# Kernel optimization log

Hardware: AMD Instinct MI355X
Metric: run time of the kernel (lower is better)

The kernel has to match this reference:

```python
import jax, jax.numpy as jnp
import numpy as np

TOKEN_DIM = 512
ATTN_DIM = 512
NUM_HEADS = 8
MLP_SIZE = 2048
EPS = 1e-6


def setup_inputs() -> dict:
    key = jax.random.key(0)
    ks = jax.random.split(key, 9)
    s_tok = 1.0 / np.sqrt(TOKEN_DIM)
    s_att = 1.0 / np.sqrt(ATTN_DIM)
    s_mlp = 1.0 / np.sqrt(MLP_SIZE)
    return {
        "inputs": jax.random.normal(ks[0], (2, 4096, TOKEN_DIM), dtype=jnp.float32),
        "Wq": jax.random.uniform(ks[1], (TOKEN_DIM, ATTN_DIM), jnp.float32, -s_tok, s_tok),
        "Wk": jax.random.uniform(ks[2], (TOKEN_DIM, ATTN_DIM), jnp.float32, -s_tok, s_tok),
        "Wv": jax.random.uniform(ks[3], (TOKEN_DIM, ATTN_DIM), jnp.float32, -s_tok, s_tok),
        "Wo": jax.random.uniform(ks[4], (ATTN_DIM, TOKEN_DIM), jnp.float32, -s_att, s_att),
        "W1": jax.random.uniform(ks[5], (TOKEN_DIM, MLP_SIZE), jnp.float32, -s_tok, s_tok),
        "b1": jax.random.uniform(ks[6], (MLP_SIZE,), jnp.float32, -s_tok, s_tok),
        "W2": jax.random.uniform(ks[7], (MLP_SIZE, TOKEN_DIM), jnp.float32, -s_mlp, s_mlp),
        "b2": jax.random.uniform(ks[8], (TOKEN_DIM,), jnp.float32, -s_mlp, s_mlp),
        "ln_att_g": jnp.ones((TOKEN_DIM,), jnp.float32),
        "ln_att_b": jnp.zeros((TOKEN_DIM,), jnp.float32),
        "ln_mlp_g": jnp.ones((TOKEN_DIM,), jnp.float32),
        "ln_mlp_b": jnp.zeros((TOKEN_DIM,), jnp.float32),
    }


def _layernorm(x, g, b):
    mu = jnp.mean(x, axis=-1, keepdims=True)
    var = jnp.mean(jnp.square(x - mu), axis=-1, keepdims=True)
    return (x - mu) * jax.lax.rsqrt(var + EPS) * g + b


def _attention(x, Wq, Wk, Wv, Wo):
    B, N, _ = x.shape
    H, Dh = NUM_HEADS, ATTN_DIM // NUM_HEADS
    # project then split heads: (B, N, H, Dh) -> (B, H, N, Dh)
    q = (x @ Wq).reshape(B, N, H, Dh).transpose(0, 2, 1, 3)
    k = (x @ Wk).reshape(B, N, H, Dh).transpose(0, 2, 1, 3)
    v = (x @ Wv).reshape(B, N, H, Dh).transpose(0, 2, 1, 3)
    scale = Dh ** -0.5
    scores = jnp.einsum("bhnd,bhmd->bhnm", q, k) * scale  # full NxN scores
    attn = jax.nn.softmax(scores, axis=-1)
    out = jnp.einsum("bhnm,bhmd->bhnd", attn, v)
    out = out.transpose(0, 2, 1, 3).reshape(B, N, ATTN_DIM)
    return out @ Wo


def reference(inputs, Wq, Wk, Wv, Wo, W1, b1, W2, b2,
              ln_att_g, ln_att_b, ln_mlp_g, ln_mlp_b):
    x = _layernorm(inputs, ln_att_g, ln_att_b)
    x = _attention(x, Wq, Wk, Wv, Wo)
    y = x + inputs
    z = _layernorm(y, ln_mlp_g, ln_mlp_b)
    z = jax.nn.gelu(z @ W1 + b1, approximate=False) @ W2 + b2
    return z + y
```

## Files before the change

### kernel.cpp

```cpp
#include <hip/hip_runtime.h>
#include <hip/hip_bf16.h>
#include <cmath>


typedef unsigned short u16;
typedef float  f32x4  __attribute__((ext_vector_type(4)));
typedef short  bf16x8 __attribute__((ext_vector_type(8)));
typedef u16    u16x4  __attribute__((ext_vector_type(4)));

#define DEV __device__ __forceinline__
#define AS1(p) ((const __attribute__((address_space(1))) void*)(p))
#define AS3(p) ((__attribute__((address_space(3))) void*)(p))

static constexpr int Mrows = 8192;
static constexpr int Dtok  = 512;
static constexpr int Fmlp  = 2048;
static constexpr float LOG2E = 1.44269504088896340736f;

DEV u16 f2b(float f) {
  union { float f; unsigned u; } v; v.f = f;
  unsigned r = v.u + 0x7fffu + ((v.u >> 16) & 1u);
  return (u16)(r >> 16);
}

DEV unsigned cvtpk(float a, float b) {
  unsigned r;
  asm("v_cvt_pk_bf16_f32 %0, %1, %2" : "=v"(r) : "v"(a), "v"(b));
  return r;
}

DEV void plswap16(unsigned &a, unsigned &b) {
  asm("v_permlane16_swap_b32 %0, %1" : "+v"(a), "+v"(b));
}

DEV float ex2(float x) {
#if __has_builtin(__builtin_amdgcn_exp2f)
  return __builtin_amdgcn_exp2f(x);
#else
  float r; asm("v_exp_f32 %0, %1" : "=v"(r) : "v"(x)); return r;
#endif
}

DEV f32x4 mfma32(bf16x8 a, bf16x8 b, f32x4 c) {
  return __builtin_amdgcn_mfma_f32_16x16x32_bf16(a, b, c, 0, 0, 0);
}

__global__ __launch_bounds__(256) void convert_all(
    const float* __restrict__ Wq, const float* __restrict__ Wk,
    const float* __restrict__ Wv, const float* __restrict__ Wo,
    const float* __restrict__ W1, const float* __restrict__ W2,
    u16* __restrict__ Wqt, u16* __restrict__ Wkt, u16* __restrict__ Wvt,
    u16* __restrict__ Wot, u16* __restrict__ W1t, u16* __restrict__ W2t,
    float qscale) {
  int bid = blockIdx.x;
  const float* src; u16* dst; int K, N; float sc = 1.0f;
  if (bid < 1024)      { src = Wq; dst = Wqt; K = 512;  N = 512;  sc = qscale; }
  else if (bid < 2048) { src = Wk; dst = Wkt; K = 512;  N = 512;  bid -= 1024; }
  else if (bid < 3072) { src = Wv; dst = Wvt; K = 512;  N = 512;  bid -= 2048; }
  else if (bid < 4096) { src = Wo; dst = Wot; K = 512;  N = 512;  bid -= 3072; }
  else if (bid < 8192) { src = W1; dst = W1t; K = 512;  N = 2048; bid -= 4096; }
  else                 { src = W2; dst = W2t; K = 2048; N = 512;  bid -= 8192; }
  const int idx = bid * 256 + threadIdx.x;
  const int k = idx / N, n = idx - k * N;
  dst[(size_t)n * K + k] = f2b(src[idx] * sc);
}

__global__ __launch_bounds__(256) void ln_kernel(const float* __restrict__ x,
                                                 const float* __restrict__ g,
                                                 const float* __restrict__ b,
                                                 u16* __restrict__ o) {
  const int row = blockIdx.x, tid = threadIdx.x;
  float2 v = ((const float2*)(x + (size_t)row * 512))[tid];
  float s = v.x + v.y, ss = v.x * v.x + v.y * v.y;
#pragma unroll
  for (int off = 32; off > 0; off >>= 1) {
    s  += __shfl_down(s, off);
    ss += __shfl_down(ss, off);
  }
  __shared__ float ps[4], pss[4];
  const int wave = tid >> 6, lane = tid & 63;
  if (lane == 0) { ps[wave] = s; pss[wave] = ss; }
  __syncthreads();
  const float S  = ps[0] + ps[1] + ps[2] + ps[3];
  const float SS = pss[0] + pss[1] + pss[2] + pss[3];
  const float mean = S * (1.0f / 512.0f);
  const float var  = SS * (1.0f / 512.0f) - mean * mean;
  const float rstd = rsqrtf(var + 1e-6f);
  const float2 gg = ((const float2*)g)[tid];
  const float2 bb = ((const float2*)b)[tid];
  ushort2 ov;
  ov.x = f2b((v.x - mean) * rstd * gg.x + bb.x);
  ov.y = f2b((v.y - mean) * rstd * gg.y + bb.y);
  ((ushort2*)(o + (size_t)row * 512))[tid] = ov;
}

template <int EPI, int BM>
__global__ __launch_bounds__(256) void gemm_kernel(
    const u16* __restrict__ A, const u16* __restrict__ Bt,
    u16* __restrict__ outb, u16* __restrict__ outbK, u16* __restrict__ outbV,
    float* __restrict__ outf,
    const float* __restrict__ bias, const float* __restrict__ resid,
    int M, int N, int K) {
  __shared__ u16 Al[BM * 32];
  __shared__ u16 Bl[128 * 32];
  constexpr int WM = BM / 2;
  const int tid = threadIdx.x;
  const int wave = tid >> 6, lane = tid & 63;
  const int lhi = lane >> 4, llo = lane & 15;
  const int wr = wave >> 1, wc = wave & 1;
  const int m0 = blockIdx.y * BM, n0 = blockIdx.x * 128;

  f32x4 acc[BM / 32][4] = {};

  for (int k0 = 0; k0 < K; k0 += 32) {
#pragma unroll
    for (int i = 0; i < BM / 64; ++i) {
      const int rb = i * 64 + wave * 16;
      const u16* sa = A + (size_t)(m0 + rb + (lane >> 2)) * K + k0 + (lane & 3) * 8;
      __builtin_amdgcn_global_load_lds(AS1(sa), AS3(&Al[rb * 32]), 16, 0, 0);
    }
#pragma unroll
    for (int i = 0; i < 2; ++i) {
      const int rb = i * 64 + wave * 16;
      const u16* sb = Bt + (size_t)(n0 + rb + (lane >> 2)) * K + k0 + (lane & 3) * 8;
      __builtin_amdgcn_global_load_lds(AS1(sb), AS3(&Bl[rb * 32]), 16, 0, 0);
    }
    __syncthreads();
    bf16x8 af[BM / 32], bfr[4];
#pragma unroll
    for (int mi = 0; mi < BM / 32; ++mi)
      af[mi] = *(const bf16x8*)&Al[(wr * WM + mi * 16 + llo) * 32 + lhi * 8];
#pragma unroll
    for (int ni = 0; ni < 4; ++ni)
      bfr[ni] = *(const bf16x8*)&Bl[(wc * 64 + ni * 16 + llo) * 32 + lhi * 8];
#pragma unroll
    for (int mi = 0; mi < BM / 32; ++mi)
#pragma unroll
      for (int ni = 0; ni < 4; ++ni)
        acc[mi][ni] = __builtin_amdgcn_mfma_f32_16x16x32_bf16(af[mi], bfr[ni],
                                                              acc[mi][ni], 0, 0, 0);
    __syncthreads();
  }

  if constexpr (EPI == 5) {
    if (n0 < 1024) {
      u16* dst = (n0 < 512) ? outb : outbK;
      const int c0 = (n0 & 511) + wc * 64;
#pragma unroll
      for (int mi = 0; mi < BM / 32; ++mi)
#pragma unroll
        for (int r = 0; r < 4; ++r) {
          const size_t grow = (size_t)m0 + wr * WM + mi * 16 + lhi * 4 + r;
#pragma unroll
          for (int ni = 0; ni < 4; ++ni)
            dst[grow * 512 + c0 + ni * 16 + llo] = f2b(acc[mi][ni][r]);
        }
    } else {
      const int bb = m0 >> 12;
      const int nb = (m0 & 4095) + wr * WM + lhi * 4;
#pragma unroll
      for (int mi = 0; mi < BM / 32; ++mi)
#pragma unroll
        for (int ni = 0; ni < 4; ++ni) {
          const int gcol = (n0 - 1024) + wc * 64 + ni * 16 + llo;
          u16x4 pk;
#pragma unroll
          for (int r = 0; r < 4; ++r) pk[r] = f2b(acc[mi][ni][r]);
          u16* dst = outbV + (((size_t)(bb * 8 + (gcol >> 6))) * 64 + (gcol & 63)) * 4096
                           + nb + mi * 16;
          *(u16x4*)dst = pk;
        }
    }
  } else {
#pragma unroll
    for (int mi = 0; mi < BM / 32; ++mi) {
#pragma unroll
      for (int r = 0; r < 4; ++r) {
        const size_t grow = (size_t)m0 + wr * WM + mi * 16 + lhi * 4 + r;
#pragma unroll
        for (int ni = 0; ni < 4; ++ni) {
          const int gcol = n0 + wc * 64 + ni * 16 + llo;
          float v = acc[mi][ni][r];
          if (EPI == 0) {
            outb[grow * N + gcol] = f2b(v);
          } else if (EPI == 1) {
            v += bias[gcol];
            v = 0.5f * v * (1.0f + erff(v * 0.70710678118654752f));
            outb[grow * N + gcol] = f2b(v);
          } else if (EPI == 2) {
            v += resid[grow * N + gcol];
            outf[grow * N + gcol] = v;
          } else {
            v += bias[gcol] + resid[grow * N + gcol];
            outf[grow * N + gcol] = v;
          }
        }
      }
    }
  }
}

__global__ __launch_bounds__(256) void attn_kernel(const u16* __restrict__ Q,
                                                   const u16* __restrict__ Kg,
                                                   const u16* __restrict__ VT,
                                                   u16* __restrict__ O) {
  const int qt = blockIdx.x, bh = blockIdx.y;
  const int b = bh >> 3, h = bh & 7;
  const int tid = threadIdx.x, wave = tid >> 6, lane = tid & 63;
  const int lhi = lane >> 4, llo = lane & 15;

  __shared__ u16 Kl[2][4096];
  __shared__ u16 Vl[2][4096];

  const size_t rowbase = (size_t)b * 4096;
  const int col0 = h * 64;
  const int q0 = qt * 128;

  bf16x8 qf0[2], qf1[2];
  {
    const u16* qp0 = Q + (rowbase + q0 + wave * 32 + llo) * 512 + col0 + lhi * 8;
    qf0[0] = *(const bf16x8*)qp0;
    qf0[1] = *(const bf16x8*)(qp0 + 32);
    const u16* qp1 = qp0 + (size_t)16 * 512;
    qf1[0] = *(const bf16x8*)qp1;
    qf1[1] = *(const bf16x8*)(qp1 + 32);
  }

  const int srow8 = lane >> 3;
  const int kcsw  = ((lane & 7) ^ srow8) * 8;
  const u16* kbase0 = Kg + (rowbase + wave * 16 + srow8) * 512 + col0 + kcsw;
  const u16* kbase1 = kbase0 + (size_t)8 * 512;
  const u16* vbase0 = VT + ((size_t)bh * 64 + wave * 16 + srow8) * 4096 + kcsw;
  const u16* vbase1 = vbase0 + (size_t)8 * 4096;

  const int xr = (llo & 7) << 4;
  const int ka0 = (16 * lhi) ^ xr;
  const int ka1 = (16 * (4 + lhi)) ^ xr;
  const int csig = ((lhi & 1) << 1) | (lhi >> 1);
  const int vb0 = 16 * (csig ^ (llo & 7));
  const int vb1 = 16 * ((csig | 4) ^ (llo & 7));

  const bf16x8 ones = {(short)0x3F80, (short)0x3F80, (short)0x3F80, (short)0x3F80,
                       (short)0x3F80, (short)0x3F80, (short)0x3F80, (short)0x3F80};

  f32x4 o0[4] = {}, o1[4] = {};
  f32x4 o40 = {}, o41 = {};

  auto stage = [&](int kvr, int B) {
    __builtin_amdgcn_global_load_lds(AS1(kbase0 + (size_t)kvr * 512),
                                     AS3(&Kl[B][wave * 1024]), 16, 0, 0);
    __builtin_amdgcn_global_load_lds(AS1(kbase1 + (size_t)kvr * 512),
                                     AS3(&Kl[B][wave * 1024 + 512]), 16, 0, 0);
    __builtin_amdgcn_global_load_lds(AS1(vbase0 + kvr),
                                     AS3(&Vl[B][wave * 1024]), 16, 0, 0);
    __builtin_amdgcn_global_load_lds(AS1(vbase1 + kvr),
                                     AS3(&Vl[B][wave * 1024 + 512]), 16, 0, 0);
  };

  auto packP = [&](const f32x4* stj, bf16x8& Bv0, bf16x8& Bv1) {
    unsigned a0 = cvtpk(ex2(stj[0][0]), ex2(stj[0][1]));
    unsigned a1 = cvtpk(ex2(stj[0][2]), ex2(stj[0][3]));
    unsigned b0 = cvtpk(ex2(stj[1][0]), ex2(stj[1][1]));
    unsigned b1 = cvtpk(ex2(stj[1][2]), ex2(stj[1][3]));
    unsigned c0 = cvtpk(ex2(stj[2][0]), ex2(stj[2][1]));
    unsigned c1 = cvtpk(ex2(stj[2][2]), ex2(stj[2][3]));
    unsigned d0 = cvtpk(ex2(stj[3][0]), ex2(stj[3][1]));
    unsigned d1 = cvtpk(ex2(stj[3][2]), ex2(stj[3][3]));
    plswap16(a0, b0); plswap16(a1, b1);
    plswap16(c0, d0); plswap16(c1, d1);
    union UB { unsigned u[4]; bf16x8 v; } X, Y;
    X.u[0] = a0; X.u[1] = a1; X.u[2] = b0; X.u[3] = b1;
    Y.u[0] = c0; Y.u[1] = c1; Y.u[2] = d0; Y.u[3] = d1;
    Bv0 = X.v; Bv1 = Y.v;
  };

  auto compute = [&](int B) {
    const char* klb = (const char*)&Kl[B][0] + llo * 128;
    const char* vlb = (const char*)&Vl[B][0] + llo * 128;
    f32x4 st0[4], st1[4];
    __builtin_amdgcn_s_setprio(1);
#pragma unroll
    for (int jt = 0; jt < 4; ++jt) {
      bf16x8 kf0 = *(const bf16x8*)(klb + jt * 2048 + ka0);
      bf16x8 kf1 = *(const bf16x8*)(klb + jt * 2048 + ka1);
      f32x4 z0 = {}, z1 = {};
      z0 = mfma32(kf0, qf0[0], z0); z0 = mfma32(kf1, qf0[1], z0);
      z1 = mfma32(kf0, qf1[0], z1); z1 = mfma32(kf1, qf1[1], z1);
      st0[jt] = z0; st1[jt] = z1;
    }
    __builtin_amdgcn_s_setprio(0);
    bf16x8 P00, P01, P10, P11;
    packP(st0, P00, P01);
    packP(st1, P10, P11);
    __builtin_amdgcn_s_setprio(1);
    o40 = mfma32(ones, P00, o40); o40 = mfma32(ones, P01, o40);
    o41 = mfma32(ones, P10, o41); o41 = mfma32(ones, P11, o41);
#pragma unroll
    for (int dt = 0; dt < 4; ++dt) {
      bf16x8 vf0 = *(const bf16x8*)(vlb + dt * 2048 + vb0);
      bf16x8 vf1 = *(const bf16x8*)(vlb + dt * 2048 + vb1);
      o0[dt] = mfma32(vf0, P00, o0[dt]); o0[dt] = mfma32(vf1, P01, o0[dt]);
      o1[dt] = mfma32(vf0, P10, o1[dt]); o1[dt] = mfma32(vf1, P11, o1[dt]);
    }
    __builtin_amdgcn_s_setprio(0);
  };

  stage(0, 0);
  __syncthreads();
  for (int kv0 = 0; kv0 < 4096; kv0 += 128) {
    stage(kv0 + 64, 1);
    compute(0);
    __syncthreads();
    if (kv0 + 128 < 4096) stage(kv0 + 128, 0);
    compute(1);
    __syncthreads();
  }

  {
    const float inv = 1.0f / o40[0];
    u16* op = O + (rowbase + q0 + wave * 32 + llo) * 512 + col0 + 4 * lhi;
#pragma unroll
    for (int dt = 0; dt < 4; ++dt) {
      u16x4 pk;
#pragma unroll
      for (int r = 0; r < 4; ++r) pk[r] = f2b(o0[dt][r] * inv);
      *(u16x4*)(op + dt * 16) = pk;
    }
  }
  {
    const float inv = 1.0f / o41[0];
    u16* op = O + (rowbase + q0 + wave * 32 + 16 + llo) * 512 + col0 + 4 * lhi;
#pragma unroll
    for (int dt = 0; dt < 4; ++dt) {
      u16x4 pk;
#pragma unroll
      for (int r = 0; r < 4; ++r) pk[r] = f2b(o1[dt][r] * inv);
      *(u16x4*)(op + dt * 16) = pk;
    }
  }
}

extern "C" void kernel_launch(void* const* d_in, const int* in_sizes, int n_in,
                              void* d_out, int out_size, void* d_ws, size_t ws_size,
                              hipStream_t stream) {
  const float* inputs = (const float*)d_in[0];
  const float* Wq  = (const float*)d_in[1];
  const float* Wk  = (const float*)d_in[2];
  const float* Wv  = (const float*)d_in[3];
  const float* Wo  = (const float*)d_in[4];
  const float* W1  = (const float*)d_in[5];
  const float* b1  = (const float*)d_in[6];
  const float* W2  = (const float*)d_in[7];
  const float* b2  = (const float*)d_in[8];
  const float* g1  = (const float*)d_in[9];
  const float* be1 = (const float*)d_in[10];
  const float* g2  = (const float*)d_in[11];
  const float* be2 = (const float*)d_in[12];
  float* out = (float*)d_out;

  const int M = Mrows, D = Dtok, F = Fmlp;

  char* w = (char*)d_ws;
  u16* xln  = (u16*)w;  w += (size_t)M * D * 2;
  u16* Qb   = (u16*)w;  w += (size_t)M * D * 2;
  u16* Kb   = (u16*)w;  w += (size_t)M * D * 2;
  u16* VT   = (u16*)w;  w += (size_t)M * D * 2;
  u16* attn = (u16*)w;  w += (size_t)M * D * 2;
  float* y  = (float*)w; w += (size_t)M * D * 4;
  u16* Wqt  = (u16*)w;  w += (size_t)D * D * 2;
  u16* Wkt  = (u16*)w;  w += (size_t)D * D * 2;
  u16* Wvt  = (u16*)w;  w += (size_t)D * D * 2;
  u16* Wot  = (u16*)w;  w += (size_t)D * D * 2;
  u16* W1t  = (u16*)w;  w += (size_t)D * F * 2;
  u16* W2t  = (u16*)w;  w += (size_t)F * D * 2;
  u16* zln = xln;
  u16* h1  = Qb;

  convert_all<<<dim3(12288), 256, 0, stream>>>(Wq, Wk, Wv, Wo, W1, W2,
                                               Wqt, Wkt, Wvt, Wot, W1t, W2t,
                                               0.125f * LOG2E);

  ln_kernel<<<dim3(M), 256, 0, stream>>>(inputs, g1, be1, xln);

  gemm_kernel<5, 128><<<dim3(12, M / 128), 256, 0, stream>>>(
      xln, Wqt, Qb, Kb, VT, nullptr, nullptr, nullptr, M, 512, D);

  attn_kernel<<<dim3(32, 16), 256, 0, stream>>>(Qb, Kb, VT, attn);

  gemm_kernel<2, 64><<<dim3(4, M / 64), 256, 0, stream>>>(
      attn, Wot, nullptr, nullptr, nullptr, y, nullptr, inputs, M, D, D);

  ln_kernel<<<dim3(M), 256, 0, stream>>>(y, g2, be2, zln);

  gemm_kernel<1, 128><<<dim3(16, M / 128), 256, 0, stream>>>(
      zln, W1t, h1, nullptr, nullptr, nullptr, b1, nullptr, M, F, D);
  gemm_kernel<3, 64><<<dim3(4, M / 64), 256, 0, stream>>>(
      h1, W2t, nullptr, nullptr, nullptr, out, b2, y, M, D, F);
}
```

Before: 243.3 us.

## Split attention KV range across two blocks and double-buffer GEMM LDS

The attention kernel now splits the 4096-key range into two halves along a third grid dimension. Each half writes unnormalized partial outputs and row denominators, and a new combine kernel sums them and normalizes. This doubles the attention grid from 512 to 1024 blocks to fill more of the GPU's compute units, at the cost of an extra launch and extra memory traffic for the partials. Separately, the GEMM kernel gains double-buffered LDS staging so the next K-slice loads while the current one computes, which doubles shared memory use.

```diff
diff --git a/kernel.cpp b/kernel.cpp
--- a/kernel.cpp
+++ b/kernel.cpp
@@ -7,6 +7,7 @@
 typedef float  f32x4  __attribute__((ext_vector_type(4)));
 typedef short  bf16x8 __attribute__((ext_vector_type(8)));
 typedef u16    u16x4  __attribute__((ext_vector_type(4)));
+typedef u16    u16x8  __attribute__((ext_vector_type(8)));
 
 #define DEV __device__ __forceinline__
 #define AS1(p) ((const __attribute__((address_space(1))) void*)(p))
@@ -21,6 +22,10 @@
   union { float f; unsigned u; } v; v.f = f;
   unsigned r = v.u + 0x7fffu + ((v.u >> 16) & 1u);
   return (u16)(r >> 16);
+}
+
+DEV float b2f(u16 x) {
+  union { unsigned u; float f; } v; v.u = ((unsigned)x) << 16; return v.f;
 }
 
 DEV unsigned cvtpk(float a, float b) {
@@ -101,8 +106,8 @@
     float* __restrict__ outf,
     const float* __restrict__ bias, const float* __restrict__ resid,
     int M, int N, int K) {
-  __shared__ u16 Al[BM * 32];
-  __shared__ u16 Bl[128 * 32];
+  __shared__ u16 Al[2][BM * 32];
+  __shared__ u16 Bl[2][128 * 32];
   constexpr int WM = BM / 2;
   const int tid = threadIdx.x;
   const int wave = tid >> 6, lane = tid & 63;
@@ -112,33 +117,45 @@
 
   f32x4 acc[BM / 32][4] = {};
 
-  for (int k0 = 0; k0 < K; k0 += 32) {
+  auto stageG = [&](int k0, int Bf) {
 #pragma unroll
     for (int i = 0; i < BM / 64; ++i) {
       const int rb = i * 64 + wave * 16;
       const u16* sa = A + (size_t)(m0 + rb + (lane >> 2)) * K + k0 + (lane & 3) * 8;
-      __builtin_amdgcn_global_load_lds(AS1(sa), AS3(&Al[rb * 32]), 16, 0, 0);
+      __builtin_amdgcn_global_load_lds(AS1(sa), AS3(&Al[Bf][rb * 32]), 16, 0, 0);
     }
 #pragma unroll
     for (int i = 0; i < 2; ++i) {
       const int rb = i * 64 + wave * 16;
       const u16* sb = Bt + (size_t)(n0 + rb + (lane >> 2)) * K + k0 + (lane & 3) * 8;
-      __builtin_amdgcn_global_load_lds(AS1(sb), AS3(&Bl[rb * 32]), 16, 0, 0);
-    }
-    __syncthreads();
+      __builtin_amdgcn_global_load_lds(AS1(sb), AS3(&Bl[Bf][rb * 32]), 16, 0, 0);
+    }
+  };
+
+  auto computeG = [&](int Bf) {
     bf16x8 af[BM / 32], bfr[4];
 #pragma unroll
     for (int mi = 0; mi < BM / 32; ++mi)
-      af[mi] = *(const bf16x8*)&Al[(wr * WM + mi * 16 + llo) * 32 + lhi * 8];
+      af[mi] = *(const bf16x8*)&Al[Bf][(wr * WM + mi * 16 + llo) * 32 + lhi * 8];
 #pragma unroll
     for (int ni = 0; ni < 4; ++ni)
-      bfr[ni] = *(const bf16x8*)&Bl[(wc * 64 + ni * 16 + llo) * 32 + lhi * 8];
+      bfr[ni] = *(const bf16x8*)&Bl[Bf][(wc * 64 + ni * 16 + llo) * 32 + lhi * 8];
 #pragma unroll
     for (int mi = 0; mi < BM / 32; ++mi)
 #pragma unroll
       for (int ni = 0; ni < 4; ++ni)
         acc[mi][ni] = __builtin_amdgcn_mfma_f32_16x16x32_bf16(af[mi], bfr[ni],
                                                               acc[mi][ni], 0, 0, 0);
+  };
+
+  stageG(0, 0);
+  __syncthreads();
+  for (int k0 = 0; k0 < K; k0 += 64) {
+    stageG(k0 + 32, 1);
+    computeG(0);
+    __syncthreads();
+    if (k0 + 64 < K) stageG(k0 + 64, 0);
+    computeG(1);
     __syncthreads();
   }
 
@@ -203,8 +220,10 @@
 __global__ __launch_bounds__(256) void attn_kernel(const u16* __restrict__ Q,
                                                    const u16* __restrict__ Kg,
                                                    const u16* __restrict__ VT,
-                                                   u16* __restrict__ O) {
-  const int qt = blockIdx.x, bh = blockIdx.y;
+                                                   u16* __restrict__ P0,
+                                                   u16* __restrict__ P1,
+                                                   float* __restrict__ den) {
+  const int qt = blockIdx.x, bh = blockIdx.y, z = blockIdx.z;
   const int b = bh >> 3, h = bh & 7;
   const int tid = threadIdx.x, wave = tid >> 6, lane = tid & 63;
   const int lhi = lane >> 4, llo = lane & 15;
@@ -215,6 +234,7 @@
   const size_t rowbase = (size_t)b * 4096;
   const int col0 = h * 64;
   const int q0 = qt * 128;
+  const int kvlo = z * 2048;
 
   bf16x8 qf0[2], qf1[2];
   {
@@ -305,39 +325,60 @@
     __builtin_amdgcn_s_setprio(0);
   };
 
-  stage(0, 0);
+  stage(kvlo, 0);
   __syncthreads();
-  for (int kv0 = 0; kv0 < 4096; kv0 += 128) {
+  for (int kv0 = kvlo; kv0 < kvlo + 2048; kv0 += 128) {
     stage(kv0 + 64, 1);
     compute(0);
     __syncthreads();
-    if (kv0 + 128 < 4096) stage(kv0 + 128, 0);
+    if (kv0 + 128 < kvlo + 2048) stage(kv0 + 128, 0);
     compute(1);
     __syncthreads();
   }
 
+  u16* P = z ? P1 : P0;
   {
-    const float inv = 1.0f / o40[0];
-    u16* op = O + (rowbase + q0 + wave * 32 + llo) * 512 + col0 + 4 * lhi;
+    const int qrow = q0 + wave * 32 + llo;
+    u16* op = P + (rowbase + qrow) * 512 + col0 + 4 * lhi;
 #pragma unroll
     for (int dt = 0; dt < 4; ++dt) {
       u16x4 pk;
 #pragma unroll
-      for (int r = 0; r < 4; ++r) pk[r] = f2b(o0[dt][r] * inv);
+      for (int r = 0; r < 4; ++r) pk[r] = f2b(o0[dt][r]);
       *(u16x4*)(op + dt * 16) = pk;
     }
+    if (lhi == 0) den[(size_t)z * 65536 + bh * 4096 + qrow] = o40[0];
   }
   {
-    const float inv = 1.0f / o41[0];
-    u16* op = O + (rowbase + q0 + wave * 32 + 16 + llo) * 512 + col0 + 4 * lhi;
+    const int qrow = q0 + wave * 32 + 16 + llo;
+    u16* op = P + (rowbase + qrow) * 512 + col0 + 4 * lhi;
 #pragma unroll
     for (int dt = 0; dt < 4; ++dt) {
       u16x4 pk;
 #pragma unroll
-      for (int r = 0; r < 4; ++r) pk[r] = f2b(o1[dt][r] * inv);
+      for (int r = 0; r < 4; ++r) pk[r] = f2b(o1[dt][r]);
       *(u16x4*)(op + dt * 16) = pk;
     }
-  }
+    if (lhi == 0) den[(size_t)z * 65536 + bh * 4096 + qrow] = o41[0];
+  }
+}
+
+__global__ __launch_bounds__(256) void attn_combine(const u16* __restrict__ P0,
+                                                    const u16* __restrict__ P1,
+                                                    const float* __restrict__ den,
+                                                    u16* __restrict__ out) {
+  const int idx = blockIdx.x * 256 + threadIdx.x;
+  const int row = idx >> 6, c0 = (idx & 63) * 8;
+  const int bq = row & 4095, bb = row >> 12, h = c0 >> 6;
+  const size_t dbase = (size_t)(bb * 8 + h) * 4096 + bq;
+  const float inv = 1.0f / (den[dbase] + den[dbase + 65536]);
+  const size_t off = (size_t)row * 512 + c0;
+  u16x8 a = *(const u16x8*)(P0 + off);
+  u16x8 b = *(const u16x8*)(P1 + off);
+  u16x8 o;
+#pragma unroll
+  for (int j = 0; j < 8; ++j) o[j] = f2b((b2f(a[j]) + b2f(b[j])) * inv);
+  *(u16x8*)(out + off) = o;
 }
 
 extern "C" void kernel_launch(void* const* d_in, const int* in_sizes, int n_in,
@@ -367,6 +408,7 @@
   u16* VT   = (u16*)w;  w += (size_t)M * D * 2;
   u16* attn = (u16*)w;  w += (size_t)M * D * 2;
   float* y  = (float*)w; w += (size_t)M * D * 4;
+  float* dn = (float*)w; w += (size_t)2 * 65536 * 4;
   u16* Wqt  = (u16*)w;  w += (size_t)D * D * 2;
   u16* Wkt  = (u16*)w;  w += (size_t)D * D * 2;
   u16* Wvt  = (u16*)w;  w += (size_t)D * D * 2;
@@ -385,7 +427,8 @@
   gemm_kernel<5, 128><<<dim3(12, M / 128), 256, 0, stream>>>(
       xln, Wqt, Qb, Kb, VT, nullptr, nullptr, nullptr, M, 512, D);
 
-  attn_kernel<<<dim3(32, 16), 256, 0, stream>>>(Qb, Kb, VT, attn);
+  attn_kernel<<<dim3(32, 16, 2), 256, 0, stream>>>(Qb, Kb, VT, xln, attn, dn);
+  attn_combine<<<dim3(2048), 256, 0, stream>>>(xln, attn, dn, attn);
 
   gemm_kernel<2, 64><<<dim3(4, M / 64), 256, 0, stream>>>(
       attn, Wot, nullptr, nullptr, nullptr, y, nullptr, inputs, M, D, D);
```

Result: no change. 243.7 us (+0.2%).

## Double-buffer GEMM LDS tiles and software-pipeline attention QK ahead of PV

Applied to the files above, without the earlier changes.

The GEMM kernel now keeps two LDS buffers for the A and B tiles and issues the global-to-LDS load for the next K slice before running the MFMAs on the current one, so load latency overlaps compute. The attention loop is restructured into a one-tile-ahead pipeline. Each iteration loads the next tile's V fragments into registers and computes its QK scores while the current tile's exp, pack and PV MFMAs run, and it also stages the tile after that. This leaves one barrier per tile and gives more independent work between LDS reads and MFMAs. The cost is higher register pressure from holding two tiles of scores and V fragments, which may reduce occupancy or cause spills.

```diff
diff --git a/kernel.cpp b/kernel.cpp
--- a/kernel.cpp
+++ b/kernel.cpp
@@ -101,8 +101,8 @@
     float* __restrict__ outf,
     const float* __restrict__ bias, const float* __restrict__ resid,
     int M, int N, int K) {
-  __shared__ u16 Al[BM * 32];
-  __shared__ u16 Bl[128 * 32];
+  __shared__ u16 Al[2][BM * 32];
+  __shared__ u16 Bl[2][128 * 32];
   constexpr int WM = BM / 2;
   const int tid = threadIdx.x;
   const int wave = tid >> 6, lane = tid & 63;
@@ -112,33 +112,45 @@
 
   f32x4 acc[BM / 32][4] = {};
 
-  for (int k0 = 0; k0 < K; k0 += 32) {
+  auto stageG = [&](int k0, int Bf) {
 #pragma unroll
     for (int i = 0; i < BM / 64; ++i) {
       const int rb = i * 64 + wave * 16;
       const u16* sa = A + (size_t)(m0 + rb + (lane >> 2)) * K + k0 + (lane & 3) * 8;
-      __builtin_amdgcn_global_load_lds(AS1(sa), AS3(&Al[rb * 32]), 16, 0, 0);
+      __builtin_amdgcn_global_load_lds(AS1(sa), AS3(&Al[Bf][rb * 32]), 16, 0, 0);
     }
 #pragma unroll
     for (int i = 0; i < 2; ++i) {
       const int rb = i * 64 + wave * 16;
       const u16* sb = Bt + (size_t)(n0 + rb + (lane >> 2)) * K + k0 + (lane & 3) * 8;
-      __builtin_amdgcn_global_load_lds(AS1(sb), AS3(&Bl[rb * 32]), 16, 0, 0);
-    }
-    __syncthreads();
+      __builtin_amdgcn_global_load_lds(AS1(sb), AS3(&Bl[Bf][rb * 32]), 16, 0, 0);
+    }
+  };
+
+  auto computeG = [&](int Bf) {
     bf16x8 af[BM / 32], bfr[4];
 #pragma unroll
     for (int mi = 0; mi < BM / 32; ++mi)
-      af[mi] = *(const bf16x8*)&Al[(wr * WM + mi * 16 + llo) * 32 + lhi * 8];
+      af[mi] = *(const bf16x8*)&Al[Bf][(wr * WM + mi * 16 + llo) * 32 + lhi * 8];
 #pragma unroll
     for (int ni = 0; ni < 4; ++ni)
-      bfr[ni] = *(const bf16x8*)&Bl[(wc * 64 + ni * 16 + llo) * 32 + lhi * 8];
+      bfr[ni] = *(const bf16x8*)&Bl[Bf][(wc * 64 + ni * 16 + llo) * 32 + lhi * 8];
 #pragma unroll
     for (int mi = 0; mi < BM / 32; ++mi)
 #pragma unroll
       for (int ni = 0; ni < 4; ++ni)
         acc[mi][ni] = __builtin_amdgcn_mfma_f32_16x16x32_bf16(af[mi], bfr[ni],
                                                               acc[mi][ni], 0, 0, 0);
+  };
+
+  stageG(0, 0);
+  __syncthreads();
+  for (int k0 = 0; k0 < K; k0 += 64) {
+    stageG(k0 + 32, 1);
+    computeG(0);
+    __syncthreads();
+    if (k0 + 64 < K) stageG(k0 + 64, 0);
+    computeG(1);
     __syncthreads();
   }
 
@@ -257,6 +269,30 @@
                                      AS3(&Vl[B][wave * 1024 + 512]), 16, 0, 0);
   };
 
+  auto loadV = [&](int B, bf16x8* v) {
+    const char* vlb = (const char*)&Vl[B][0] + llo * 128;
+#pragma unroll
+    for (int dt = 0; dt < 4; ++dt) {
+      v[2 * dt]     = *(const bf16x8*)(vlb + dt * 2048 + vb0);
+      v[2 * dt + 1] = *(const bf16x8*)(vlb + dt * 2048 + vb1);
+    }
+  };
+
+  auto qk = [&](int B, f32x4* s0, f32x4* s1) {
+    const char* klb = (const char*)&Kl[B][0] + llo * 128;
+    __builtin_amdgcn_s_setprio(1);
+#pragma unroll
+    for (int jt = 0; jt < 4; ++jt) {
+      bf16x8 kf0 = *(const bf16x8*)(klb + jt * 2048 + ka0);
+      bf16x8 kf1 = *(const bf16x8*)(klb + jt * 2048 + ka1);
+      f32x4 z0 = {}, z1 = {};
+      z0 = mfma32(kf0, qf0[0], z0); z0 = mfma32(kf1, qf0[1], z0);
+      z1 = mfma32(kf0, qf1[0], z1); z1 = mfma32(kf1, qf1[1], z1);
+      s0[jt] = z0; s1[jt] = z1;
+    }
+    __builtin_amdgcn_s_setprio(0);
+  };
+
   auto packP = [&](const f32x4* stj, bf16x8& Bv0, bf16x8& Bv1) {
     unsigned a0 = cvtpk(ex2(stj[0][0]), ex2(stj[0][1]));
     unsigned a1 = cvtpk(ex2(stj[0][2]), ex2(stj[0][3]));
@@ -274,46 +310,44 @@
     Bv0 = X.v; Bv1 = Y.v;
   };
 
-  auto compute = [&](int B) {
-    const char* klb = (const char*)&Kl[B][0] + llo * 128;
-    const char* vlb = (const char*)&Vl[B][0] + llo * 128;
-    f32x4 st0[4], st1[4];
-    __builtin_amdgcn_s_setprio(1);
-#pragma unroll
-    for (int jt = 0; jt < 4; ++jt) {
-      bf16x8 kf0 = *(const bf16x8*)(klb + jt * 2048 + ka0);
-      bf16x8 kf1 = *(const bf16x8*)(klb + jt * 2048 + ka1);
-      f32x4 z0 = {}, z1 = {};
-      z0 = mfma32(kf0, qf0[0], z0); z0 = mfma32(kf1, qf0[1], z0);
-      z1 = mfma32(kf0, qf1[0], z1); z1 = mfma32(kf1, qf1[1], z1);
-      st0[jt] = z0; st1[jt] = z1;
-    }
-    __builtin_amdgcn_s_setprio(0);
+  stage(0, 0);
+  __syncthreads();
+  bf16x8 vP[8];
+  f32x4 stP0[4], stP1[4];
+  loadV(0, vP);
+  qk(0, stP0, stP1);
+  stage(64, 1);
+
+  for (int t = 0; t < 64; ++t) {
+    const int cur = t & 1, nxt = cur ^ 1;
+    __syncthreads();
+    bf16x8 vN[8];
+    f32x4 stN0[4], stN1[4];
+    if (t < 63) {
+      loadV(nxt, vN);
+      qk(nxt, stN0, stN1);
+      if (t < 62) stage((t + 2) * 64, cur);
+    }
     bf16x8 P00, P01, P10, P11;
-    packP(st0, P00, P01);
-    packP(st1, P10, P11);
+    packP(stP0, P00, P01);
+    packP(stP1, P10, P11);
     __builtin_amdgcn_s_setprio(1);
     o40 = mfma32(ones, P00, o40); o40 = mfma32(ones, P01, o40);
     o41 = mfma32(ones, P10, o41); o41 = mfma32(ones, P11, o41);
 #pragma unroll
     for (int dt = 0; dt < 4; ++dt) {
-      bf16x8 vf0 = *(const bf16x8*)(vlb + dt * 2048 + vb0);
-      bf16x8 vf1 = *(const bf16x8*)(vlb + dt * 2048 + vb1);
-      o0[dt] = mfma32(vf0, P00, o0[dt]); o0[dt] = mfma32(vf1, P01, o0[dt]);
-      o1[dt] = mfma32(vf0, P10, o1[dt]); o1[dt] = mfma32(vf1, P11, o1[dt]);
+      o0[dt] = mfma32(vP[2 * dt], P00, o0[dt]);
+      o0[dt] = mfma32(vP[2 * dt + 1], P01, o0[dt]);
+      o1[dt] = mfma32(vP[2 * dt], P10, o1[dt]);
+      o1[dt] = mfma32(vP[2 * dt + 1], P11, o1[dt]);
     }
     __builtin_amdgcn_s_setprio(0);
-  };
-
-  stage(0, 0);
-  __syncthreads();
-  for (int kv0 = 0; kv0 < 4096; kv0 += 128) {
-    stage(kv0 + 64, 1);
-    compute(0);
-    __syncthreads();
-    if (kv0 + 128 < 4096) stage(kv0 + 128, 0);
-    compute(1);
-    __syncthreads();
+    if (t < 63) {
+#pragma unroll
+      for (int i = 0; i < 8; ++i) vP[i] = vN[i];
+#pragma unroll
+      for (int j = 0; j < 4; ++j) { stP0[j] = stN0[j]; stP1[j] = stN1[j]; }
+    }
   }
 
   {
```

New measurement: 235.5 us. 1.03x faster.

## Triple-buffer LDS staging in GEMM and attention with one vmcnt-gated barrier

Applied to the files above, without the earlier changes.

The GEMM and attention kernels now use three LDS buffers instead of one or two. Global-to-LDS loads are issued two steps ahead, and each iteration waits with a partial s_waitcnt vmcnt followed by a single s_barrier, replacing two __syncthreads per step. The aim is to hide global load latency behind MFMA work and halve the barrier count. The cost is more LDS per block, which may lower occupancy, and reliance on hand-counted vmcnt values that must match the number of loads each stage issues.

```diff
diff --git a/kernel.cpp b/kernel.cpp
--- a/kernel.cpp
+++ b/kernel.cpp
@@ -44,6 +44,8 @@
 DEV f32x4 mfma32(bf16x8 a, bf16x8 b, f32x4 c) {
   return __builtin_amdgcn_mfma_f32_16x16x32_bf16(a, b, c, 0, 0, 0);
 }
+
+#define WAIT_BARRIER(N) asm volatile("s_waitcnt vmcnt(" #N ")\n\ts_barrier" ::: "memory")
 
 __global__ __launch_bounds__(256) void convert_all(
     const float* __restrict__ Wq, const float* __restrict__ Wk,
@@ -101,8 +103,8 @@
     float* __restrict__ outf,
     const float* __restrict__ bias, const float* __restrict__ resid,
     int M, int N, int K) {
-  __shared__ u16 Al[BM * 32];
-  __shared__ u16 Bl[128 * 32];
+  __shared__ u16 Al[3 * BM * 32];
+  __shared__ u16 Bl[3 * 128 * 32];
   constexpr int WM = BM / 2;
   const int tid = threadIdx.x;
   const int wave = tid >> 6, lane = tid & 63;
@@ -112,34 +114,53 @@
 
   f32x4 acc[BM / 32][4] = {};
 
-  for (int k0 = 0; k0 < K; k0 += 32) {
+  auto stageG = [&](int k0, int buf) {
 #pragma unroll
     for (int i = 0; i < BM / 64; ++i) {
       const int rb = i * 64 + wave * 16;
       const u16* sa = A + (size_t)(m0 + rb + (lane >> 2)) * K + k0 + (lane & 3) * 8;
-      __builtin_amdgcn_global_load_lds(AS1(sa), AS3(&Al[rb * 32]), 16, 0, 0);
+      __builtin_amdgcn_global_load_lds(AS1(sa), AS3(&Al[buf * (BM * 32) + rb * 32]), 16, 0, 0);
     }
 #pragma unroll
     for (int i = 0; i < 2; ++i) {
       const int rb = i * 64 + wave * 16;
       const u16* sb = Bt + (size_t)(n0 + rb + (lane >> 2)) * K + k0 + (lane & 3) * 8;
-      __builtin_amdgcn_global_load_lds(AS1(sb), AS3(&Bl[rb * 32]), 16, 0, 0);
-    }
-    __syncthreads();
+      __builtin_amdgcn_global_load_lds(AS1(sb), AS3(&Bl[buf * (128 * 32) + rb * 32]), 16, 0, 0);
+    }
+  };
+
+  auto computeG = [&](int buf) {
+    const u16* Ab = &Al[buf * (BM * 32)];
+    const u16* Bb = &Bl[buf * (128 * 32)];
     bf16x8 af[BM / 32], bfr[4];
 #pragma unroll
     for (int mi = 0; mi < BM / 32; ++mi)
-      af[mi] = *(const bf16x8*)&Al[(wr * WM + mi * 16 + llo) * 32 + lhi * 8];
+      af[mi] = *(const bf16x8*)&Ab[(wr * WM + mi * 16 + llo) * 32 + lhi * 8];
 #pragma unroll
     for (int ni = 0; ni < 4; ++ni)
-      bfr[ni] = *(const bf16x8*)&Bl[(wc * 64 + ni * 16 + llo) * 32 + lhi * 8];
+      bfr[ni] = *(const bf16x8*)&Bb[(wc * 64 + ni * 16 + llo) * 32 + lhi * 8];
 #pragma unroll
     for (int mi = 0; mi < BM / 32; ++mi)
 #pragma unroll
       for (int ni = 0; ni < 4; ++ni)
         acc[mi][ni] = __builtin_amdgcn_mfma_f32_16x16x32_bf16(af[mi], bfr[ni],
                                                               acc[mi][ni], 0, 0, 0);
-    __syncthreads();
+  };
+
+  const int nsteps = K >> 5;
+  stageG(0, 0);
+  stageG(32, 1);
+  int cur = 0, nx1 = 1, nx2 = 2;
+  for (int t = 0; t < nsteps; ++t) {
+    if (t < nsteps - 1) {
+      if constexpr (BM == 128) WAIT_BARRIER(4);
+      else                     WAIT_BARRIER(3);
+    } else {
+      WAIT_BARRIER(0);
+    }
+    if (t + 2 < nsteps) stageG((t + 2) * 32, nx2);
+    computeG(cur);
+    const int tmp = cur; cur = nx1; nx1 = nx2; nx2 = tmp;
   }
 
   if constexpr (EPI == 5) {
@@ -209,8 +230,8 @@
   const int tid = threadIdx.x, wave = tid >> 6, lane = tid & 63;
   const int lhi = lane >> 4, llo = lane & 15;
 
-  __shared__ u16 Kl[2][4096];
-  __shared__ u16 Vl[2][4096];
+  __shared__ u16 Kl[3 * 4096];
+  __shared__ u16 Vl[3 * 4096];
 
   const size_t rowbase = (size_t)b * 4096;
   const int col0 = h * 64;
@@ -246,15 +267,15 @@
   f32x4 o0[4] = {}, o1[4] = {};
   f32x4 o40 = {}, o41 = {};
 
-  auto stage = [&](int kvr, int B) {
+  auto stage = [&](int kvr, int buf) {
     __builtin_amdgcn_global_load_lds(AS1(kbase0 + (size_t)kvr * 512),
-                                     AS3(&Kl[B][wave * 1024]), 16, 0, 0);
+                                     AS3(&Kl[buf * 4096 + wave * 1024]), 16, 0, 0);
     __builtin_amdgcn_global_load_lds(AS1(kbase1 + (size_t)kvr * 512),
-                                     AS3(&Kl[B][wave * 1024 + 512]), 16, 0, 0);
+                                     AS3(&Kl[buf * 4096 + wave * 1024 + 512]), 16, 0, 0);
     __builtin_amdgcn_global_load_lds(AS1(vbase0 + kvr),
-                                     AS3(&Vl[B][wave * 1024]), 16, 0, 0);
+                                     AS3(&Vl[buf * 4096 + wave * 1024]), 16, 0, 0);
     __builtin_amdgcn_global_load_lds(AS1(vbase1 + kvr),
-                                     AS3(&Vl[B][wave * 1024 + 512]), 16, 0, 0);
+                                     AS3(&Vl[buf * 4096 + wave * 1024 + 512]), 16, 0, 0);
   };
 
   auto packP = [&](const f32x4* stj, bf16x8& Bv0, bf16x8& Bv1) {
@@ -274,9 +295,9 @@
     Bv0 = X.v; Bv1 = Y.v;
   };
 
-  auto compute = [&](int B) {
-    const char* klb = (const char*)&Kl[B][0] + llo * 128;
-    const char* vlb = (const char*)&Vl[B][0] + llo * 128;
+  auto compute = [&](int buf) {
+    const char* klb = (const char*)&Kl[buf * 4096] + llo * 128;
+    const char* vlb = (const char*)&Vl[buf * 4096] + llo * 128;
     f32x4 st0[4], st1[4];
     __builtin_amdgcn_s_setprio(1);
 #pragma unroll
@@ -306,14 +327,14 @@
   };
 
   stage(0, 0);
-  __syncthreads();
-  for (int kv0 = 0; kv0 < 4096; kv0 += 128) {
-    stage(kv0 + 64, 1);
-    compute(0);
-    __syncthreads();
-    if (kv0 + 128 < 4096) stage(kv0 + 128, 0);
-    compute(1);
-    __syncthreads();
+  stage(64, 1);
+  int cur = 0, nx1 = 1, nx2 = 2;
+  for (int t = 0; t < 64; ++t) {
+    if (t < 63) WAIT_BARRIER(4);
+    else        WAIT_BARRIER(0);
+    if (t + 2 < 64) stage((t + 2) * 64, nx2);
+    compute(cur);
+    const int tmp = cur; cur = nx1; nx1 = nx2; nx2 = tmp;
   }
 
   {
```

Measured after the change: 246.6 us. Within noise of the previous version (+1.4%).
